# Kernel optimization log

Measured on AMD Instinct MI355X. Metric: run time of the kernel, lower is better.

The kernel has to match this reference:

```python
import jax, jax.numpy as jnp
import numpy as np

NUM_LEVELS = 4
N = 524288


def _e8_roots() -> np.ndarray:
    """The 240 roots of the E8 lattice, float32 [240, 8].

    Type 1 (112): all permutations of (+-1, +-1, 0^6).
    Type 2 (128): (+-1/2)^8 with an even number of minus signs.
    """
    roots = []
    for i in range(8):
        for j in range(i + 1, 8):
            for si in (1.0, -1.0):
                for sj in (1.0, -1.0):
                    v = np.zeros(8, dtype=np.float64)
                    v[i] = si
                    v[j] = sj
                    roots.append(v)
    for m in range(256):
        signs = np.array([1.0 if ((m >> k) & 1) == 0 else -1.0 for k in range(8)])
        if int((signs < 0).sum()) % 2 == 0:
            roots.append(0.5 * signs)
    out = np.stack(roots).astype(np.float32)
    assert out.shape == (240, 8)
    return out


def setup_inputs() -> dict:
    key = jax.random.key(0)
    x = jax.random.normal(key, (N, 8), dtype=jnp.float32)
    roots = jnp.asarray(_e8_roots())  # [240, 8] fixed codebook (buffer)
    return {"x": x, "roots": roots}


def reference(x, roots):
    # Residual multi-level nearest-neighbor quantization against E8 roots.
    x_flat = x.reshape(-1, 8)                       # [N, 8]
    r2 = jnp.sum(roots * roots, axis=1)[None, :]    # [1, 240]
    qsum = jnp.zeros_like(x_flat)
    residual = x_flat
    indices = []
    for _level in range(NUM_LEVELS):
        res2 = jnp.sum(residual * residual, axis=1, keepdims=True)      # [N, 1]
        # squared euclidean distances, clamped at 0 for numerical safety
        d2 = jnp.clip(res2 + r2 - 2.0 * (residual @ roots.T), 0.0)      # [N, 240]
        idx = jnp.argmin(d2, axis=-1)                                   # [N]
        qsum = qsum + roots[idx]                                        # gather
        residual = x_flat - qsum
        indices.append(idx)
    quantized = qsum.reshape(x.shape)
    # straight-through estimator: value == quantized, grad flows via x
    quantized_ste = quantized + x - jax.lax.stop_gradient(x)
    qerr = jnp.mean(
        (jax.lax.stop_gradient(x) - jax.lax.stop_gradient(quantized)) ** 2
    )
    idx_stack = jnp.stack(indices).reshape((NUM_LEVELS,) + x.shape[:-1])
    return quantized_ste, idx_stack, qerr
```

## Files before the change

kernel.cpp:

```cpp
#include <hip/hip_runtime.h>
#include <math.h>


__global__ __launch_bounds__(256) void e8_quant_kernel(
    const float* __restrict__ x, const float* __restrict__ roots,
    float* __restrict__ out, float* __restrict__ partials, int nrow) {
#pragma clang fp contract(off)
  __shared__ float lroots[240 * 8];
  __shared__ float wred0[4];
  __shared__ float wred1[4];
  for (int t = threadIdx.x; t < 240 * 8; t += 256) lroots[t] = roots[t];
  __syncthreads();

  const int row0 = blockIdx.x * 512 + threadIdx.x;
  const int row1 = row0 + 256;
  const bool act0 = row0 < nrow;
  const bool act1 = row1 < nrow;
  float* out_idx = out + (size_t)nrow * 8;

  float xr0[8], qs0[8], r0[8];
  float xr1[8], qs1[8], r1[8];
  float e0 = 0.f, e1 = 0.f;

  if (act0) {
    const float4 xa = *(const float4*)(x + (size_t)row0 * 8);
    const float4 xb = *(const float4*)(x + (size_t)row0 * 8 + 4);
    xr0[0] = xa.x; xr0[1] = xa.y; xr0[2] = xa.z; xr0[3] = xa.w;
    xr0[4] = xb.x; xr0[5] = xb.y; xr0[6] = xb.z; xr0[7] = xb.w;
#pragma unroll
    for (int k = 0; k < 8; ++k) { qs0[k] = 0.f; r0[k] = xr0[k]; }
  }
  if (act1) {
    const float4 xa = *(const float4*)(x + (size_t)row1 * 8);
    const float4 xb = *(const float4*)(x + (size_t)row1 * 8 + 4);
    xr1[0] = xa.x; xr1[1] = xa.y; xr1[2] = xa.z; xr1[3] = xa.w;
    xr1[4] = xb.x; xr1[5] = xb.y; xr1[6] = xb.z; xr1[7] = xb.w;
#pragma unroll
    for (int k = 0; k < 8; ++k) { qs1[k] = 0.f; r1[k] = xr1[k]; }
  }

  auto level_step = [&](int lvl, float (&xr)[8], float (&qs)[8],
                        float (&r)[8], int row) {
    float q[8];
#pragma unroll
    for (int k = 0; k < 8; ++k) q[k] = r[k] * r[k];
    const float res2 = ((q[0] + q[1]) + (q[2] + q[3])) +
                       ((q[4] + q[5]) + (q[6] + q[7]));
    const float s = res2 + 2.0f;

    float mg[8];
    int sb[8];
#pragma unroll
    for (int k = 0; k < 8; ++k) {
      const unsigned u = __float_as_uint(r[k]);
      mg[k] = __uint_as_float(u & 0x7fffffffu);
      sb[k] = (int)(u >> 31);
    }
    const int msk = sb[0] | (sb[1] << 1) | (sb[2] << 2) | (sb[3] << 3) |
                    (sb[4] << 4) | (sb[5] << 5) | (sb[6] << 6) | (sb[7] << 7);
    const int par = __popc(msk) & 1;
    const float Sabs = ((mg[0] + mg[1]) + (mg[2] + mg[3])) +
                       ((mg[4] + mg[5]) + (mg[6] + mg[7]));

    const int K0 = 0 | (sb[0] << 3), K1 = 1 | (sb[1] << 3),
              K2 = 2 | (sb[2] << 3), K3 = 3 | (sb[3] << 3),
              K4 = 4 | (sb[4] << 3), K5 = 5 | (sb[5] << 3),
              K6 = 6 | (sb[6] << 3), K7 = 7 | (sb[7] << 3);

    const bool g01 = mg[1] > mg[0];
    const float h01 = fmaxf(mg[0], mg[1]), l01 = fminf(mg[0], mg[1]);
    const int hk01 = g01 ? K1 : K0, lk01 = g01 ? K0 : K1;
    const bool g23 = mg[3] > mg[2];
    const float h23 = fmaxf(mg[2], mg[3]), l23 = fminf(mg[2], mg[3]);
    const int hk23 = g23 ? K3 : K2, lk23 = g23 ? K2 : K3;
    const bool g45 = mg[5] > mg[4];
    const float h45 = fmaxf(mg[4], mg[5]), l45 = fminf(mg[4], mg[5]);
    const int hk45 = g45 ? K5 : K4, lk45 = g45 ? K4 : K5;
    const bool g67 = mg[7] > mg[6];
    const float h67 = fmaxf(mg[6], mg[7]), l67 = fminf(mg[6], mg[7]);
    const int hk67 = g67 ? K7 : K6, lk67 = g67 ? K6 : K7;
    const bool qg0 = h23 > h01;
    const float qh0 = fmaxf(h01, h23);
    const int qhk0 = qg0 ? hk23 : hk01;
    const float sA0 = qg0 ? l23 : l01;
    const int sAk0 = qg0 ? lk23 : lk01;
    const float sB0 = qg0 ? h01 : h23;
    const int sBk0 = qg0 ? hk01 : hk23;
    const float loL0 = qg0 ? l01 : l23;
    const bool qx0 = sB0 > sA0;
    const float qs0v = fmaxf(sA0, sB0);
    const int qsk0 = qx0 ? sBk0 : sAk0;
    const float qt0 = qx0 ? fmaxf(sA0, loL0) : sB0;
    const bool qg1 = h67 > h45;
    const float qh1 = fmaxf(h45, h67);
    const int qhk1 = qg1 ? hk67 : hk45;
    const float sA1 = qg1 ? l67 : l45;
    const int sAk1 = qg1 ? lk67 : lk45;
    const float sB1 = qg1 ? h45 : h67;
    const int sBk1 = qg1 ? hk45 : hk67;
    const float loL1 = qg1 ? l45 : l67;
    const bool qx1 = sB1 > sA1;
    const float qs1v = fmaxf(sA1, sB1);
    const int qsk1 = qx1 ? sBk1 : sAk1;
    const float qt1 = qx1 ? fmaxf(sA1, loL1) : sB1;
    const bool fg = qh1 > qh0;
    const float A1v = fmaxf(qh0, qh1);
    const int A1K = fg ? qhk1 : qhk0;
    const float fA = fg ? qs1v : qs0v;
    const int fAk = fg ? qsk1 : qsk0;
    const float fB = fg ? qh0 : qh1;
    const int fBk = fg ? qhk0 : qhk1;
    const float tW = fg ? qt1 : qt0;
    const float sL = fg ? qs0v : qs1v;
    const bool fh = fB > fA;
    const float A2v = fmaxf(fA, fB);
    const int A2K = fh ? fBk : fAk;
    const float A3v = fh ? fmaxf(fA, sL) : fmaxf(tW, fB);

    const bool n0 = l23 < l01;
    const float mn0 = fminf(l01, l23);
    const int mnk0 = n0 ? lk23 : lk01;
    const float pr0 = n0 ? h23 : h01;
    const float ot0 = fmaxf(l01, l23);
    const bool n1 = l67 < l45;
    const float mn1 = fminf(l45, l67);
    const int mnk1 = n1 ? lk67 : lk45;
    const float pr1 = n1 ? h67 : h45;
    const float ot1 = fmaxf(l45, l67);
    const bool nf = mn1 < mn0;
    const float Aminv = fminf(mn0, mn1);
    const int AminK = nf ? mnk1 : mnk0;
    const float prW = nf ? pr1 : pr0;
    const float otW = nf ? ot1 : ot0;
    const float mnL = fmaxf(mn0, mn1);
    const float Amin2v = fminf(prW, fminf(otW, mnL));

    const float dT1r = A1v + A2v;
    const float halfS = 0.5f * Sabs;
    const float dT2 = par ? (halfS - Aminv) : halfS;

    const int p1 = A1K & 7, p2 = A2K & 7;
    const int s1b = A1K >> 3, s2b = A2K >> 3;
    const bool o12 = p1 < p2;
    const int imn = o12 ? p1 : p2, jmx = o12 ? p2 : p1;
    const int sIb = o12 ? s1b : s2b, sJb = o12 ? s2b : s1b;
    const int pbase = imn * 7 - ((imn * (imn - 1)) >> 1) + (jmx - imn - 1);
    const int t1idx = (pbase << 2) | (sIb << 1) | sJb;

    const int mp = AminK & 7;
    const int mf = par ? (msk ^ (1 << mp)) : msk;
    const int t2idx = 112 + (mf >> 1);

    const float thr = (res2 + 2.0f * Sabs + 2.0f) * 0x1.0p-20f;
    const bool a1 = (A2v - A3v) > thr;
    const bool a2 = par ? ((Amin2v - Aminv) > thr)
                        : ((Aminv + Amin2v) > thr);
    const bool c = fabsf(dT1r - dT2) > thr;

    float d1 = fmaf(-2.f, dT1r, s);
    int i1 = t1idx;
    float d2x = 0.f;
    int i2 = t2idx;

    if (__any(!a1)) {
      if (!a1) {
        if (Aminv > thr) {
          float best = 3.4028235e38f;
          int bidx = 0;
          int ci = 0;
#pragma unroll
          for (int i = 0; i < 8; ++i) {
#pragma unroll
            for (int j = i + 1; j < 8; ++j) {
              const float aa = mg[i] + mg[j];
              const float d = fmaf(-2.f, aa, s);
              const int idx = (ci << 2) | (sb[i] << 1) | sb[j];
              if (d < best) { best = d; bidx = idx; }
              ++ci;
            }
          }
          d1 = best;
          i1 = bidx;
        } else {
          float best = 3.4028235e38f;
          int be = 0;
          int ci = 0;
#pragma unroll
          for (int i = 0; i < 8; ++i) {
#pragma unroll
            for (int j = i + 1; j < 8; ++j) {
              const float a = r[i] + r[j];
              const float b = r[i] - r[j];
              float d;
              d = fmaf(-2.f, a, s);
              if (d < best) { best = d; be = ci + 0; }
              d = fmaf(-2.f, b, s);
              if (d < best) { best = d; be = ci + 1; }
              d = fmaf(2.f, b, s);
              if (d < best) { best = d; be = ci + 2; }
              d = fmaf(2.f, a, s);
              if (d < best) { best = d; be = ci + 3; }
              ci += 4;
            }
          }
          d1 = best;
          i1 = be;
        }
      }
    }

    if (__any(!a2)) {
      if (!a2) {
        float h[8];
#pragma unroll
        for (int k = 0; k < 8; ++k) h[k] = 0.5f * r[k];
        const bool cheap = par && ((Amin2v + Amin2v) > thr);
        if (cheap) {
          float best2 = 3.4028235e38f;
          int bt = 0;
#pragma unroll
          for (int k = 0; k < 8; ++k) {
            const int mk = msk ^ (1 << k);
            float v = (mk & 1) ? -h[0] : h[0];
#pragma unroll
            for (int j = 1; j < 8; ++j)
              v = (mk & (1 << j)) ? (v - h[j]) : (v + h[j]);
            const float d = fmaf(-2.f, v, s);
            const int t = mk >> 1;
            const bool take = (d < best2) || (d == best2 && t < bt);
            best2 = take ? d : best2;
            bt = take ? t : bt;
          }
          d2x = best2;
          i2 = 112 + bt;
        } else {
          float best2 = 3.4028235e38f;
          int bt = 0;
#pragma unroll 1
          for (int t = 0; t < 128; ++t) {
            const int m = (t << 1) | (__popc(t) & 1);
            float v = (m & 1) ? -h[0] : h[0];
#pragma unroll
            for (int j = 1; j < 8; ++j)
              v = (m & (1 << j)) ? (v - h[j]) : (v + h[j]);
            const float d = fmaf(-2.f, v, s);
            if (d < best2) { best2 = d; bt = t; }
          }
          d2x = best2;
          i2 = 112 + bt;
        }
      }
    }

    if (__any(!c && a2)) {
      if (!c && a2) {
        const int flip = par ? mp : 8;
        float v = (flip == 0) ? -(0.5f * mg[0]) : (0.5f * mg[0]);
#pragma unroll
        for (int j = 1; j < 8; ++j) {
          const float tj = 0.5f * mg[j];
          v = (flip == j) ? (v - tj) : (v + tj);
        }
        d2x = fmaf(-2.f, v, s);
      }
    }

    const int bi = c ? ((dT1r > dT2) ? i1 : i2)
                     : ((d1 <= d2x) ? i1 : i2);

    out_idx[(size_t)lvl * nrow + row] = (float)bi;

    const float4 ra = *(const float4*)(lroots + bi * 8);
    const float4 rb = *(const float4*)(lroots + bi * 8 + 4);
    qs[0] += ra.x; qs[1] += ra.y; qs[2] += ra.z; qs[3] += ra.w;
    qs[4] += rb.x; qs[5] += rb.y; qs[6] += rb.z; qs[7] += rb.w;
#pragma unroll
    for (int k = 0; k < 8; ++k) r[k] = xr[k] - qs[k];
  };

#pragma unroll 1
  for (int lvl = 0; lvl < 4; ++lvl) {
    if (act0) level_step(lvl, xr0, qs0, r0, row0);
    if (act1) level_step(lvl, xr1, qs1, r1, row1);
  }

  if (act0) {
    float o[8];
#pragma unroll
    for (int k = 0; k < 8; ++k) o[k] = (qs0[k] + xr0[k]) - xr0[k];
    *(float4*)(out + (size_t)row0 * 8) = make_float4(o[0], o[1], o[2], o[3]);
    *(float4*)(out + (size_t)row0 * 8 + 4) =
        make_float4(o[4], o[5], o[6], o[7]);
#pragma unroll
    for (int k = 0; k < 8; ++k) e0 = fmaf(r0[k], r0[k], e0);
  }
  if (act1) {
    float o[8];
#pragma unroll
    for (int k = 0; k < 8; ++k) o[k] = (qs1[k] + xr1[k]) - xr1[k];
    *(float4*)(out + (size_t)row1 * 8) = make_float4(o[0], o[1], o[2], o[3]);
    *(float4*)(out + (size_t)row1 * 8 + 4) =
        make_float4(o[4], o[5], o[6], o[7]);
#pragma unroll
    for (int k = 0; k < 8; ++k) e1 = fmaf(r1[k], r1[k], e1);
  }

#pragma unroll
  for (int off = 32; off > 0; off >>= 1) e0 += __shfl_down(e0, off, 64);
#pragma unroll
  for (int off = 32; off > 0; off >>= 1) e1 += __shfl_down(e1, off, 64);
  const int lane = threadIdx.x & 63, wv = threadIdx.x >> 6;
  if (lane == 0) { wred0[wv] = e0; wred1[wv] = e1; }
  __syncthreads();
  if (threadIdx.x == 0) {
    partials[2 * blockIdx.x] =
        (wred0[0] + wred0[1]) + (wred0[2] + wred0[3]);
    partials[2 * blockIdx.x + 1] =
        (wred1[0] + wred1[1]) + (wred1[2] + wred1[3]);
  }
}

__global__ __launch_bounds__(256) void qerr_reduce_kernel(
    const float* __restrict__ partials, float* __restrict__ out, int n,
    size_t pos, float scale) {
#pragma clang fp contract(off)
  __shared__ float wred[4];
  float e = 0.f;
  for (int i = threadIdx.x; i < n; i += 256) e += partials[i];
#pragma unroll
  for (int off = 32; off > 0; off >>= 1) e += __shfl_down(e, off, 64);
  const int lane = threadIdx.x & 63, wv = threadIdx.x >> 6;
  if (lane == 0) wred[wv] = e;
  __syncthreads();
  if (threadIdx.x == 0)
    out[pos] = ((wred[0] + wred[1]) + (wred[2] + wred[3])) * scale;
}

extern "C" void kernel_launch(void* const* d_in, const int* in_sizes, int n_in,
                              void* d_out, int out_size, void* d_ws,
                              size_t ws_size, hipStream_t stream) {
  const float* x = (const float*)d_in[0];
  const float* roots = (const float*)d_in[1];
  float* out = (float*)d_out;
  float* partials = (float*)d_ws;

  const int nrow = in_sizes[0] / 8;
  const int nblocks = (nrow + 511) / 512;

  e8_quant_kernel<<<nblocks, 256, 0, stream>>>(x, roots, out, partials, nrow);

  const size_t qerr_pos = (size_t)nrow * 12;
  const float scale = 1.0f / (float)((size_t)nrow * 8);
  qerr_reduce_kernel<<<1, 256, 0, stream>>>(partials, out, 2 * nblocks,
                                            qerr_pos, scale);
}
```

Measured before the change: 90.28 us.

## Drop shared-memory codebook and rebuild chosen root arithmetically, merging both rows' slow paths

```diff
diff --git a/kernel.cpp b/kernel.cpp
--- a/kernel.cpp
+++ b/kernel.cpp
@@ -6,317 +6,348 @@
     const float* __restrict__ x, const float* __restrict__ roots,
     float* __restrict__ out, float* __restrict__ partials, int nrow) {
 #pragma clang fp contract(off)
-  __shared__ float lroots[240 * 8];
-  __shared__ float wred0[4];
-  __shared__ float wred1[4];
-  for (int t = threadIdx.x; t < 240 * 8; t += 256) lroots[t] = roots[t];
-  __syncthreads();
+  __shared__ float wredA[4];
+  __shared__ float wredB[4];
 
   const int row0 = blockIdx.x * 512 + threadIdx.x;
   const int row1 = row0 + 256;
-  const bool act0 = row0 < nrow;
-  const bool act1 = row1 < nrow;
+  const bool act[2] = {row0 < nrow, row1 < nrow};
+  const int rl[2] = {act[0] ? row0 : nrow - 1, act[1] ? row1 : nrow - 1};
   float* out_idx = out + (size_t)nrow * 8;
-
-  float xr0[8], qs0[8], r0[8];
-  float xr1[8], qs1[8], r1[8];
-  float e0 = 0.f, e1 = 0.f;
-
-  if (act0) {
-    const float4 xa = *(const float4*)(x + (size_t)row0 * 8);
-    const float4 xb = *(const float4*)(x + (size_t)row0 * 8 + 4);
-    xr0[0] = xa.x; xr0[1] = xa.y; xr0[2] = xa.z; xr0[3] = xa.w;
-    xr0[4] = xb.x; xr0[5] = xb.y; xr0[6] = xb.z; xr0[7] = xb.w;
-#pragma unroll
-    for (int k = 0; k < 8; ++k) { qs0[k] = 0.f; r0[k] = xr0[k]; }
+  float* op[2] = {out_idx + row0, out_idx + row1};
+
+  float xr[2][8], qs[2][8], rr[2][8];
+#pragma unroll
+  for (int sl = 0; sl < 2; ++sl) {
+    const float4 xa = *(const float4*)(x + (size_t)rl[sl] * 8);
+    const float4 xb = *(const float4*)(x + (size_t)rl[sl] * 8 + 4);
+    xr[sl][0] = xa.x; xr[sl][1] = xa.y; xr[sl][2] = xa.z; xr[sl][3] = xa.w;
+    xr[sl][4] = xb.x; xr[sl][5] = xb.y; xr[sl][6] = xb.z; xr[sl][7] = xb.w;
+#pragma unroll
+    for (int k = 0; k < 8; ++k) { qs[sl][k] = 0.f; rr[sl][k] = xr[sl][k]; }
   }
-  if (act1) {
-    const float4 xa = *(const float4*)(x + (size_t)row1 * 8);
-    const float4 xb = *(const float4*)(x + (size_t)row1 * 8 + 4);
-    xr1[0] = xa.x; xr1[1] = xa.y; xr1[2] = xa.z; xr1[3] = xa.w;
-    xr1[4] = xb.x; xr1[5] = xb.y; xr1[6] = xb.z; xr1[7] = xb.w;
-#pragma unroll
-    for (int k = 0; k < 8; ++k) { qs1[k] = 0.f; r1[k] = xr1[k]; }
-  }
-
-  auto level_step = [&](int lvl, float (&xr)[8], float (&qs)[8],
-                        float (&r)[8], int row) {
-    float q[8];
-#pragma unroll
-    for (int k = 0; k < 8; ++k) q[k] = r[k] * r[k];
-    const float res2 = ((q[0] + q[1]) + (q[2] + q[3])) +
-                       ((q[4] + q[5]) + (q[6] + q[7]));
-    const float s = res2 + 2.0f;
-
-    float mg[8];
-    int sb[8];
-#pragma unroll
-    for (int k = 0; k < 8; ++k) {
-      const unsigned u = __float_as_uint(r[k]);
-      mg[k] = __uint_as_float(u & 0x7fffffffu);
-      sb[k] = (int)(u >> 31);
+
+#pragma unroll 1
+  for (int lvl = 0; lvl < 4; ++lvl) {
+    float s_[2], thr_[2], dT1_[2], dT2_[2], Amn_[2], Amn2_[2];
+    int t1_[2], t2_[2], pk_[2], bi_[2];
+    bool a1_[2], a2_[2], c_[2], fell_[2], pT1_[2];
+
+#pragma unroll
+    for (int sl = 0; sl < 2; ++sl) {
+      float q[8];
+#pragma unroll
+      for (int k = 0; k < 8; ++k) q[k] = rr[sl][k] * rr[sl][k];
+      const float res2 = ((q[0] + q[1]) + (q[2] + q[3])) +
+                         ((q[4] + q[5]) + (q[6] + q[7]));
+      const float s = res2 + 2.0f;
+
+      float mg[8];
+      int sb[8];
+#pragma unroll
+      for (int k = 0; k < 8; ++k) {
+        const unsigned u = __float_as_uint(rr[sl][k]);
+        mg[k] = __uint_as_float(u & 0x7fffffffu);
+        sb[k] = (int)(u >> 31);
+      }
+      const int msk = sb[0] | (sb[1] << 1) | (sb[2] << 2) | (sb[3] << 3) |
+                      (sb[4] << 4) | (sb[5] << 5) | (sb[6] << 6) |
+                      (sb[7] << 7);
+      const int par = __popc(msk) & 1;
+      const float Sabs = ((mg[0] + mg[1]) + (mg[2] + mg[3])) +
+                         ((mg[4] + mg[5]) + (mg[6] + mg[7]));
+
+      const int K0 = 0 | (sb[0] << 3), K1 = 1 | (sb[1] << 3),
+                K2 = 2 | (sb[2] << 3), K3 = 3 | (sb[3] << 3),
+                K4 = 4 | (sb[4] << 3), K5 = 5 | (sb[5] << 3),
+                K6 = 6 | (sb[6] << 3), K7 = 7 | (sb[7] << 3);
+
+      const bool g01 = mg[1] > mg[0];
+      const float h01 = fmaxf(mg[0], mg[1]), l01 = fminf(mg[0], mg[1]);
+      const int hk01 = g01 ? K1 : K0, lk01 = g01 ? K0 : K1;
+      const bool g23 = mg[3] > mg[2];
+      const float h23 = fmaxf(mg[2], mg[3]), l23 = fminf(mg[2], mg[3]);
+      const int hk23 = g23 ? K3 : K2, lk23 = g23 ? K2 : K3;
+      const bool g45 = mg[5] > mg[4];
+      const float h45 = fmaxf(mg[4], mg[5]), l45 = fminf(mg[4], mg[5]);
+      const int hk45 = g45 ? K5 : K4, lk45 = g45 ? K4 : K5;
+      const bool g67 = mg[7] > mg[6];
+      const float h67 = fmaxf(mg[6], mg[7]), l67 = fminf(mg[6], mg[7]);
+      const int hk67 = g67 ? K7 : K6, lk67 = g67 ? K6 : K7;
+      const bool qg0 = h23 > h01;
+      const float qh0 = fmaxf(h01, h23);
+      const int qhk0 = qg0 ? hk23 : hk01;
+      const float sA0 = qg0 ? l23 : l01;
+      const int sAk0 = qg0 ? lk23 : lk01;
+      const float sB0 = qg0 ? h01 : h23;
+      const int sBk0 = qg0 ? hk01 : hk23;
+      const float loL0 = qg0 ? l01 : l23;
+      const bool qx0 = sB0 > sA0;
+      const float qs0v = fmaxf(sA0, sB0);
+      const int qsk0 = qx0 ? sBk0 : sAk0;
+      const float qt0 = qx0 ? fmaxf(sA0, loL0) : sB0;
+      const bool qg1 = h67 > h45;
+      const float qh1 = fmaxf(h45, h67);
+      const int qhk1 = qg1 ? hk67 : hk45;
+      const float sA1 = qg1 ? l67 : l45;
+      const int sAk1 = qg1 ? lk67 : lk45;
+      const float sB1 = qg1 ? h45 : h67;
+      const int sBk1 = qg1 ? hk45 : hk67;
+      const float loL1 = qg1 ? l45 : l67;
+      const bool qx1 = sB1 > sA1;
+      const float qs1v = fmaxf(sA1, sB1);
+      const int qsk1 = qx1 ? sBk1 : sAk1;
+      const float qt1 = qx1 ? fmaxf(sA1, loL1) : sB1;
+      const bool fg = qh1 > qh0;
+      const float A1v = fmaxf(qh0, qh1);
+      const int A1K = fg ? qhk1 : qhk0;
+      const float fA = fg ? qs1v : qs0v;
+      const int fAk = fg ? qsk1 : qsk0;
+      const float fB = fg ? qh0 : qh1;
+      const int fBk = fg ? qhk0 : qhk1;
+      const float tW = fg ? qt1 : qt0;
+      const float sL = fg ? qs0v : qs1v;
+      const bool fh = fB > fA;
+      const float A2v = fmaxf(fA, fB);
+      const int A2K = fh ? fBk : fAk;
+      const float A3v = fh ? fmaxf(fA, sL) : fmaxf(tW, fB);
+
+      const bool n0 = l23 < l01;
+      const float mn0 = fminf(l01, l23);
+      const int mnk0 = n0 ? lk23 : lk01;
+      const float pr0 = n0 ? h23 : h01;
+      const float ot0 = fmaxf(l01, l23);
+      const bool n1 = l67 < l45;
+      const float mn1 = fminf(l45, l67);
+      const int mnk1 = n1 ? lk67 : lk45;
+      const float pr1 = n1 ? h67 : h45;
+      const float ot1 = fmaxf(l45, l67);
+      const bool nf = mn1 < mn0;
+      const float Aminv = fminf(mn0, mn1);
+      const int AminK = nf ? mnk1 : mnk0;
+      const float prW = nf ? pr1 : pr0;
+      const float otW = nf ? ot1 : ot0;
+      const float mnL = fmaxf(mn0, mn1);
+      const float Amin2v = fminf(prW, fminf(otW, mnL));
+
+      const float dT1r = A1v + A2v;
+      const float halfS = 0.5f * Sabs;
+      const float dT2 = par ? (halfS - Aminv) : halfS;
+
+      const int p1 = A1K & 7, p2 = A2K & 7;
+      const int s1b = A1K >> 3, s2b = A2K >> 3;
+      const bool o12 = p1 < p2;
+      const int imn = o12 ? p1 : p2, jmx = o12 ? p2 : p1;
+      const int sIb = o12 ? s1b : s2b, sJb = o12 ? s2b : s1b;
+      const int pbase = imn * 7 - ((imn * (imn - 1)) >> 1) + (jmx - imn - 1);
+      const int t1idx = (pbase << 2) | (sIb << 1) | sJb;
+
+      const int mp = AminK & 7;
+      const int mf = par ? (msk ^ (1 << mp)) : msk;
+      const int t2idx = 112 + (mf >> 1);
+
+      const float thr = (res2 + 2.0f * Sabs + 2.0f) * 0x1.0p-20f;
+      const bool a1 = (A2v - A3v) > thr;
+      const bool a2 = par ? ((Amin2v - Aminv) > thr)
+                          : ((Aminv + Amin2v) > thr);
+      const bool c = fabsf(dT1r - dT2) > thr;
+
+      const int one = (1 << imn) | (1 << jmx);
+      const int sm1 = (sIb << imn) | (sJb << jmx);
+
+      s_[sl] = s; thr_[sl] = thr; dT1_[sl] = dT1r; dT2_[sl] = dT2;
+      Amn_[sl] = Aminv; Amn2_[sl] = Amin2v;
+      t1_[sl] = t1idx; t2_[sl] = t2idx;
+      pk_[sl] = one | (sm1 << 8) | (mf << 16) | (mp << 24);
+      a1_[sl] = a1; a2_[sl] = a2; c_[sl] = c;
+      const bool pT1 = dT1r > dT2;
+      pT1_[sl] = pT1;
+      bi_[sl] = pT1 ? t1idx : t2idx;
+      fell_[sl] = false;
     }
-    const int msk = sb[0] | (sb[1] << 1) | (sb[2] << 2) | (sb[3] << 3) |
-                    (sb[4] << 4) | (sb[5] << 5) | (sb[6] << 6) | (sb[7] << 7);
-    const int par = __popc(msk) & 1;
-    const float Sabs = ((mg[0] + mg[1]) + (mg[2] + mg[3])) +
-                       ((mg[4] + mg[5]) + (mg[6] + mg[7]));
-
-    const int K0 = 0 | (sb[0] << 3), K1 = 1 | (sb[1] << 3),
-              K2 = 2 | (sb[2] << 3), K3 = 3 | (sb[3] << 3),
-              K4 = 4 | (sb[4] << 3), K5 = 5 | (sb[5] << 3),
-              K6 = 6 | (sb[6] << 3), K7 = 7 | (sb[7] << 3);
-
-    const bool g01 = mg[1] > mg[0];
-    const float h01 = fmaxf(mg[0], mg[1]), l01 = fminf(mg[0], mg[1]);
-    const int hk01 = g01 ? K1 : K0, lk01 = g01 ? K0 : K1;
-    const bool g23 = mg[3] > mg[2];
-    const float h23 = fmaxf(mg[2], mg[3]), l23 = fminf(mg[2], mg[3]);
-    const int hk23 = g23 ? K3 : K2, lk23 = g23 ? K2 : K3;
-    const bool g45 = mg[5] > mg[4];
-    const float h45 = fmaxf(mg[4], mg[5]), l45 = fminf(mg[4], mg[5]);
-    const int hk45 = g45 ? K5 : K4, lk45 = g45 ? K4 : K5;
-    const bool g67 = mg[7] > mg[6];
-    const float h67 = fmaxf(mg[6], mg[7]), l67 = fminf(mg[6], mg[7]);
-    const int hk67 = g67 ? K7 : K6, lk67 = g67 ? K6 : K7;
-    const bool qg0 = h23 > h01;
-    const float qh0 = fmaxf(h01, h23);
-    const int qhk0 = qg0 ? hk23 : hk01;
-    const float sA0 = qg0 ? l23 : l01;
-    const int sAk0 = qg0 ? lk23 : lk01;
-    const float sB0 = qg0 ? h01 : h23;
-    const int sBk0 = qg0 ? hk01 : hk23;
-    const float loL0 = qg0 ? l01 : l23;
-    const bool qx0 = sB0 > sA0;
-    const float qs0v = fmaxf(sA0, sB0);
-    const int qsk0 = qx0 ? sBk0 : sAk0;
-    const float qt0 = qx0 ? fmaxf(sA0, loL0) : sB0;
-    const bool qg1 = h67 > h45;
-    const float qh1 = fmaxf(h45, h67);
-    const int qhk1 = qg1 ? hk67 : hk45;
-    const float sA1 = qg1 ? l67 : l45;
-    const int sAk1 = qg1 ? lk67 : lk45;
-    const float sB1 = qg1 ? h45 : h67;
-    const int sBk1 = qg1 ? hk45 : hk67;
-    const float loL1 = qg1 ? l45 : l67;
-    const bool qx1 = sB1 > sA1;
-    const float qs1v = fmaxf(sA1, sB1);
-    const int qsk1 = qx1 ? sBk1 : sAk1;
-    const float qt1 = qx1 ? fmaxf(sA1, loL1) : sB1;
-    const bool fg = qh1 > qh0;
-    const float A1v = fmaxf(qh0, qh1);
-    const int A1K = fg ? qhk1 : qhk0;
-    const float fA = fg ? qs1v : qs0v;
-    const int fAk = fg ? qsk1 : qsk0;
-    const float fB = fg ? qh0 : qh1;
-    const int fBk = fg ? qhk0 : qhk1;
-    const float tW = fg ? qt1 : qt0;
-    const float sL = fg ? qs0v : qs1v;
-    const bool fh = fB > fA;
-    const float A2v = fmaxf(fA, fB);
-    const int A2K = fh ? fBk : fAk;
-    const float A3v = fh ? fmaxf(fA, sL) : fmaxf(tW, fB);
-
-    const bool n0 = l23 < l01;
-    const float mn0 = fminf(l01, l23);
-    const int mnk0 = n0 ? lk23 : lk01;
-    const float pr0 = n0 ? h23 : h01;
-    const float ot0 = fmaxf(l01, l23);
-    const bool n1 = l67 < l45;
-    const float mn1 = fminf(l45, l67);
-    const int mnk1 = n1 ? lk67 : lk45;
-    const float pr1 = n1 ? h67 : h45;
-    const float ot1 = fmaxf(l45, l67);
-    const bool nf = mn1 < mn0;
-    const float Aminv = fminf(mn0, mn1);
-    const int AminK = nf ? mnk1 : mnk0;
-    const float prW = nf ? pr1 : pr0;
-    const float otW = nf ? ot1 : ot0;
-    const float mnL = fmaxf(mn0, mn1);
-    const float Amin2v = fminf(prW, fminf(otW, mnL));
-
-    const float dT1r = A1v + A2v;
-    const float halfS = 0.5f * Sabs;
-    const float dT2 = par ? (halfS - Aminv) : halfS;
-
-    const int p1 = A1K & 7, p2 = A2K & 7;
-    const int s1b = A1K >> 3, s2b = A2K >> 3;
-    const bool o12 = p1 < p2;
-    const int imn = o12 ? p1 : p2, jmx = o12 ? p2 : p1;
-    const int sIb = o12 ? s1b : s2b, sJb = o12 ? s2b : s1b;
-    const int pbase = imn * 7 - ((imn * (imn - 1)) >> 1) + (jmx - imn - 1);
-    const int t1idx = (pbase << 2) | (sIb << 1) | sJb;
-
-    const int mp = AminK & 7;
-    const int mf = par ? (msk ^ (1 << mp)) : msk;
-    const int t2idx = 112 + (mf >> 1);
-
-    const float thr = (res2 + 2.0f * Sabs + 2.0f) * 0x1.0p-20f;
-    const bool a1 = (A2v - A3v) > thr;
-    const bool a2 = par ? ((Amin2v - Aminv) > thr)
-                        : ((Aminv + Amin2v) > thr);
-    const bool c = fabsf(dT1r - dT2) > thr;
-
-    float d1 = fmaf(-2.f, dT1r, s);
-    int i1 = t1idx;
-    float d2x = 0.f;
-    int i2 = t2idx;
-
-    if (__any(!a1)) {
-      if (!a1) {
-        if (Aminv > thr) {
-          float best = 3.4028235e38f;
-          int bidx = 0;
-          int ci = 0;
-#pragma unroll
-          for (int i = 0; i < 8; ++i) {
-#pragma unroll
-            for (int j = i + 1; j < 8; ++j) {
-              const float aa = mg[i] + mg[j];
-              const float d = fmaf(-2.f, aa, s);
-              const int idx = (ci << 2) | (sb[i] << 1) | sb[j];
-              if (d < best) { best = d; bidx = idx; }
-              ++ci;
+
+    const bool slowAny = (!a1_[0]) | (!a2_[0]) | (!c_[0]) |
+                         (!a1_[1]) | (!a2_[1]) | (!c_[1]);
+    if (__any(slowAny)) {
+#pragma unroll
+      for (int sl = 0; sl < 2; ++sl) {
+        const bool slow = (!a1_[sl]) | (!a2_[sl]) | (!c_[sl]);
+        if (slow) {
+          float mg[8], h[8];
+          int sb[8];
+#pragma unroll
+          for (int k = 0; k < 8; ++k) {
+            const unsigned u = __float_as_uint(rr[sl][k]);
+            mg[k] = __uint_as_float(u & 0x7fffffffu);
+            sb[k] = (int)(u >> 31);
+            h[k] = 0.5f * rr[sl][k];
+          }
+          const int msk = sb[0] | (sb[1] << 1) | (sb[2] << 2) |
+                          (sb[3] << 3) | (sb[4] << 4) | (sb[5] << 5) |
+                          (sb[6] << 6) | (sb[7] << 7);
+          const int par = __popc(msk) & 1;
+          const float s = s_[sl];
+
+          float d1v = fmaf(-2.f, dT1_[sl], s);
+          int i1v = t1_[sl];
+          if (!a1_[sl]) {
+            if (Amn_[sl] > thr_[sl]) {
+              float best = 3.4028235e38f;
+              int bidx = 0, ci = 0;
+#pragma unroll 1
+              for (int i = 0; i < 8; ++i) {
+#pragma unroll 1
+                for (int j = i + 1; j < 8; ++j) {
+                  const float aa = mg[i] + mg[j];
+                  const float d = fmaf(-2.f, aa, s);
+                  const int idx = (ci << 2) | (sb[i] << 1) | sb[j];
+                  if (d < best) { best = d; bidx = idx; }
+                  ++ci;
+                }
+              }
+              d1v = best; i1v = bidx;
+            } else {
+              float best = 3.4028235e38f;
+              int be = 0, ci = 0;
+#pragma unroll 1
+              for (int i = 0; i < 8; ++i) {
+#pragma unroll 1
+                for (int j = i + 1; j < 8; ++j) {
+                  const float a = rr[sl][i] + rr[sl][j];
+                  const float b = rr[sl][i] - rr[sl][j];
+                  float d;
+                  d = fmaf(-2.f, a, s);
+                  if (d < best) { best = d; be = ci + 0; }
+                  d = fmaf(-2.f, b, s);
+                  if (d < best) { best = d; be = ci + 1; }
+                  d = fmaf(2.f, b, s);
+                  if (d < best) { best = d; be = ci + 2; }
+                  d = fmaf(2.f, a, s);
+                  if (d < best) { best = d; be = ci + 3; }
+                  ci += 4;
+                }
+              }
+              d1v = best; i1v = be;
             }
           }
-          d1 = best;
-          i1 = bidx;
-        } else {
-          float best = 3.4028235e38f;
-          int be = 0;
-          int ci = 0;
-#pragma unroll
-          for (int i = 0; i < 8; ++i) {
-#pragma unroll
-            for (int j = i + 1; j < 8; ++j) {
-              const float a = r[i] + r[j];
-              const float b = r[i] - r[j];
-              float d;
-              d = fmaf(-2.f, a, s);
-              if (d < best) { best = d; be = ci + 0; }
-              d = fmaf(-2.f, b, s);
-              if (d < best) { best = d; be = ci + 1; }
-              d = fmaf(2.f, b, s);
-              if (d < best) { best = d; be = ci + 2; }
-              d = fmaf(2.f, a, s);
-              if (d < best) { best = d; be = ci + 3; }
-              ci += 4;
+
+          float d2v = 0.f;
+          int i2v = t2_[sl];
+          if (!a2_[sl]) {
+            const bool cheap = par && ((Amn2_[sl] + Amn2_[sl]) > thr_[sl]);
+            if (cheap) {
+              float best2 = 3.4028235e38f;
+              int bt = 0;
+#pragma unroll 1
+              for (int k = 0; k < 8; ++k) {
+                const int mk = msk ^ (1 << k);
+                float v = (mk & 1) ? -h[0] : h[0];
+#pragma unroll
+                for (int j = 1; j < 8; ++j)
+                  v = (mk & (1 << j)) ? (v - h[j]) : (v + h[j]);
+                const float d = fmaf(-2.f, v, s);
+                const int t = mk >> 1;
+                const bool take = (d < best2) || (d == best2 && t < bt);
+                best2 = take ? d : best2;
+                bt = take ? t : bt;
+              }
+              d2v = best2; i2v = 112 + bt;
+            } else {
+              float best2 = 3.4028235e38f;
+              int bt = 0;
+#pragma unroll 1
+              for (int t = 0; t < 128; ++t) {
+                const int m = (t << 1) | (__popc(t) & 1);
+                float v = (m & 1) ? -h[0] : h[0];
+#pragma unroll
+                for (int j = 1; j < 8; ++j)
+                  v = (m & (1 << j)) ? (v - h[j]) : (v + h[j]);
+                const float d = fmaf(-2.f, v, s);
+                if (d < best2) { best2 = d; bt = t; }
+              }
+              d2v = best2; i2v = 112 + bt;
             }
+          } else if (!c_[sl]) {
+            const int mp = (pk_[sl] >> 24) & 7;
+            const int flip = par ? mp : 8;
+            float v = (flip == 0) ? -(0.5f * mg[0]) : (0.5f * mg[0]);
+#pragma unroll
+            for (int j = 1; j < 8; ++j) {
+              const float tj = 0.5f * mg[j];
+              v = (flip == j) ? (v - tj) : (v + tj);
+            }
+            d2v = fmaf(-2.f, v, s);
           }
-          d1 = best;
-          i1 = be;
+
+          const bool pT1 = c_[sl] ? (dT1_[sl] > dT2_[sl]) : (d1v <= d2v);
+          pT1_[sl] = pT1;
+          bi_[sl] = pT1 ? i1v : i2v;
+          const bool fl = (!a1_[sl]) | (!a2_[sl]);
+          fell_[sl] = fl;
+          if (fl) {
+            const float4 ra = *(const float4*)(roots + (size_t)bi_[sl] * 8);
+            const float4 rb =
+                *(const float4*)(roots + (size_t)bi_[sl] * 8 + 4);
+            qs[sl][0] += ra.x; qs[sl][1] += ra.y;
+            qs[sl][2] += ra.z; qs[sl][3] += ra.w;
+            qs[sl][4] += rb.x; qs[sl][5] += rb.y;
+            qs[sl][6] += rb.z; qs[sl][7] += rb.w;
+#pragma unroll
+            for (int k = 0; k < 8; ++k) rr[sl][k] = xr[sl][k] - qs[sl][k];
+          }
         }
       }
     }
 
-    if (__any(!a2)) {
-      if (!a2) {
-        float h[8];
-#pragma unroll
-        for (int k = 0; k < 8; ++k) h[k] = 0.5f * r[k];
-        const bool cheap = par && ((Amin2v + Amin2v) > thr);
-        if (cheap) {
-          float best2 = 3.4028235e38f;
-          int bt = 0;
-#pragma unroll
-          for (int k = 0; k < 8; ++k) {
-            const int mk = msk ^ (1 << k);
-            float v = (mk & 1) ? -h[0] : h[0];
-#pragma unroll
-            for (int j = 1; j < 8; ++j)
-              v = (mk & (1 << j)) ? (v - h[j]) : (v + h[j]);
-            const float d = fmaf(-2.f, v, s);
-            const int t = mk >> 1;
-            const bool take = (d < best2) || (d == best2 && t < bt);
-            best2 = take ? d : best2;
-            bt = take ? t : bt;
-          }
-          d2x = best2;
-          i2 = 112 + bt;
-        } else {
-          float best2 = 3.4028235e38f;
-          int bt = 0;
-#pragma unroll 1
-          for (int t = 0; t < 128; ++t) {
-            const int m = (t << 1) | (__popc(t) & 1);
-            float v = (m & 1) ? -h[0] : h[0];
-#pragma unroll
-            for (int j = 1; j < 8; ++j)
-              v = (m & (1 << j)) ? (v - h[j]) : (v + h[j]);
-            const float d = fmaf(-2.f, v, s);
-            if (d < best2) { best2 = d; bt = t; }
-          }
-          d2x = best2;
-          i2 = 112 + bt;
+#pragma unroll
+    for (int sl = 0; sl < 2; ++sl) {
+      if (act[sl]) *op[sl] = (float)bi_[sl];
+      op[sl] += nrow;
+      if (!fell_[sl]) {
+        const int one = pk_[sl] & 0xFF;
+        const int sm1 = (pk_[sl] >> 8) & 0xFF;
+        const int mfv = (pk_[sl] >> 16) & 0xFF;
+#pragma unroll
+        for (int k = 0; k < 8; ++k) {
+          const float t1r =
+              ((one >> k) & 1) ? (((sm1 >> k) & 1) ? -1.f : 1.f) : 0.f;
+          const float t2r = ((mfv >> k) & 1) ? -0.5f : 0.5f;
+          qs[sl][k] += pT1_[sl] ? t1r : t2r;
         }
+#pragma unroll
+        for (int k = 0; k < 8; ++k) rr[sl][k] = xr[sl][k] - qs[sl][k];
       }
     }
-
-    if (__any(!c && a2)) {
-      if (!c && a2) {
-        const int flip = par ? mp : 8;
-        float v = (flip == 0) ? -(0.5f * mg[0]) : (0.5f * mg[0]);
-#pragma unroll
-        for (int j = 1; j < 8; ++j) {
-          const float tj = 0.5f * mg[j];
-          v = (flip == j) ? (v - tj) : (v + tj);
-        }
-        d2x = fmaf(-2.f, v, s);
-      }
+  }
+
+  float e[2] = {0.f, 0.f};
+#pragma unroll
+  for (int sl = 0; sl < 2; ++sl) {
+    if (act[sl]) {
+      float o[8];
+#pragma unroll
+      for (int k = 0; k < 8; ++k) o[k] = (qs[sl][k] + xr[sl][k]) - xr[sl][k];
+      const int rw = sl ? row1 : row0;
+      *(float4*)(out + (size_t)rw * 8) = make_float4(o[0], o[1], o[2], o[3]);
+      *(float4*)(out + (size_t)rw * 8 + 4) =
+          make_float4(o[4], o[5], o[6], o[7]);
+#pragma unroll
+      for (int k = 0; k < 8; ++k) e[sl] = fmaf(rr[sl][k], rr[sl][k], e[sl]);
     }
-
-    const int bi = c ? ((dT1r > dT2) ? i1 : i2)
-                     : ((d1 <= d2x) ? i1 : i2);
-
-    out_idx[(size_t)lvl * nrow + row] = (float)bi;
-
-    const float4 ra = *(const float4*)(lroots + bi * 8);
-    const float4 rb = *(const float4*)(lroots + bi * 8 + 4);
-    qs[0] += ra.x; qs[1] += ra.y; qs[2] += ra.z; qs[3] += ra.w;
-    qs[4] += rb.x; qs[5] += rb.y; qs[6] += rb.z; qs[7] += rb.w;
-#pragma unroll
-    for (int k = 0; k < 8; ++k) r[k] = xr[k] - qs[k];
-  };
-
-#pragma unroll 1
-  for (int lvl = 0; lvl < 4; ++lvl) {
-    if (act0) level_step(lvl, xr0, qs0, r0, row0);
-    if (act1) level_step(lvl, xr1, qs1, r1, row1);
   }
 
-  if (act0) {
-    float o[8];
-#pragma unroll
-    for (int k = 0; k < 8; ++k) o[k] = (qs0[k] + xr0[k]) - xr0[k];
-    *(float4*)(out + (size_t)row0 * 8) = make_float4(o[0], o[1], o[2], o[3]);
-    *(float4*)(out + (size_t)row0 * 8 + 4) =
-        make_float4(o[4], o[5], o[6], o[7]);
-#pragma unroll
-    for (int k = 0; k < 8; ++k) e0 = fmaf(r0[k], r0[k], e0);
-  }
-  if (act1) {
-    float o[8];
-#pragma unroll
-    for (int k = 0; k < 8; ++k) o[k] = (qs1[k] + xr1[k]) - xr1[k];
-    *(float4*)(out + (size_t)row1 * 8) = make_float4(o[0], o[1], o[2], o[3]);
-    *(float4*)(out + (size_t)row1 * 8 + 4) =
-        make_float4(o[4], o[5], o[6], o[7]);
-#pragma unroll
-    for (int k = 0; k < 8; ++k) e1 = fmaf(r1[k], r1[k], e1);
-  }
-
+  float e0 = e[0], e1 = e[1];
 #pragma unroll
   for (int off = 32; off > 0; off >>= 1) e0 += __shfl_down(e0, off, 64);
 #pragma unroll
   for (int off = 32; off > 0; off >>= 1) e1 += __shfl_down(e1, off, 64);
   const int lane = threadIdx.x & 63, wv = threadIdx.x >> 6;
-  if (lane == 0) { wred0[wv] = e0; wred1[wv] = e1; }
+  if (lane == 0) { wredA[wv] = e0; wredB[wv] = e1; }
   __syncthreads();
   if (threadIdx.x == 0) {
-    partials[2 * blockIdx.x] =
-        (wred0[0] + wred0[1]) + (wred0[2] + wred0[3]);
+    partials[2 * blockIdx.x] = (wredA[0] + wredA[1]) + (wredA[2] + wredA[3]);
     partials[2 * blockIdx.x + 1] =
-        (wred1[0] + wred1[1]) + (wred1[2] + wred1[3]);
+        (wredB[0] + wredB[1]) + (wredB[2] + wredB[3]);
   }
 }
 
```

New measurement: 97.78 us. 8.3% more time.

## Process one row per thread and drop shared-memory roots table

Applied to the files above, without the earlier changes.

```diff
diff --git a/kernel.cpp b/kernel.cpp
--- a/kernel.cpp
+++ b/kernel.cpp
@@ -6,44 +6,28 @@
     const float* __restrict__ x, const float* __restrict__ roots,
     float* __restrict__ out, float* __restrict__ partials, int nrow) {
 #pragma clang fp contract(off)
-  __shared__ float lroots[240 * 8];
-  __shared__ float wred0[4];
-  __shared__ float wred1[4];
-  for (int t = threadIdx.x; t < 240 * 8; t += 256) lroots[t] = roots[t];
-  __syncthreads();
-
-  const int row0 = blockIdx.x * 512 + threadIdx.x;
-  const int row1 = row0 + 256;
-  const bool act0 = row0 < nrow;
-  const bool act1 = row1 < nrow;
+  __shared__ float wred[4];
+
+  const int row = blockIdx.x * 256 + threadIdx.x;
+  const bool act = row < nrow;
+  const int rl = act ? row : nrow - 1;
   float* out_idx = out + (size_t)nrow * 8;
 
-  float xr0[8], qs0[8], r0[8];
-  float xr1[8], qs1[8], r1[8];
-  float e0 = 0.f, e1 = 0.f;
-
-  if (act0) {
-    const float4 xa = *(const float4*)(x + (size_t)row0 * 8);
-    const float4 xb = *(const float4*)(x + (size_t)row0 * 8 + 4);
-    xr0[0] = xa.x; xr0[1] = xa.y; xr0[2] = xa.z; xr0[3] = xa.w;
-    xr0[4] = xb.x; xr0[5] = xb.y; xr0[6] = xb.z; xr0[7] = xb.w;
-#pragma unroll
-    for (int k = 0; k < 8; ++k) { qs0[k] = 0.f; r0[k] = xr0[k]; }
+  float xr[8], qs[8], rr[8];
+  {
+    const float4 xa = *(const float4*)(x + (size_t)rl * 8);
+    const float4 xb = *(const float4*)(x + (size_t)rl * 8 + 4);
+    xr[0] = xa.x; xr[1] = xa.y; xr[2] = xa.z; xr[3] = xa.w;
+    xr[4] = xb.x; xr[5] = xb.y; xr[6] = xb.z; xr[7] = xb.w;
+#pragma unroll
+    for (int k = 0; k < 8; ++k) { qs[k] = 0.f; rr[k] = xr[k]; }
   }
-  if (act1) {
-    const float4 xa = *(const float4*)(x + (size_t)row1 * 8);
-    const float4 xb = *(const float4*)(x + (size_t)row1 * 8 + 4);
-    xr1[0] = xa.x; xr1[1] = xa.y; xr1[2] = xa.z; xr1[3] = xa.w;
-    xr1[4] = xb.x; xr1[5] = xb.y; xr1[6] = xb.z; xr1[7] = xb.w;
-#pragma unroll
-    for (int k = 0; k < 8; ++k) { qs1[k] = 0.f; r1[k] = xr1[k]; }
-  }
-
-  auto level_step = [&](int lvl, float (&xr)[8], float (&qs)[8],
-                        float (&r)[8], int row) {
+
+#pragma unroll 1
+  for (int lvl = 0; lvl < 4; ++lvl) {
     float q[8];
 #pragma unroll
-    for (int k = 0; k < 8; ++k) q[k] = r[k] * r[k];
+    for (int k = 0; k < 8; ++k) q[k] = rr[k] * rr[k];
     const float res2 = ((q[0] + q[1]) + (q[2] + q[3])) +
                        ((q[4] + q[5]) + (q[6] + q[7]));
     const float s = res2 + 2.0f;
@@ -52,7 +36,7 @@
     int sb[8];
 #pragma unroll
     for (int k = 0; k < 8; ++k) {
-      const unsigned u = __float_as_uint(r[k]);
+      const unsigned u = __float_as_uint(rr[k]);
       mg[k] = __uint_as_float(u & 0x7fffffffu);
       sb[k] = (int)(u >> 31);
     }
@@ -157,167 +141,154 @@
                         : ((Aminv + Amin2v) > thr);
     const bool c = fabsf(dT1r - dT2) > thr;
 
-    float d1 = fmaf(-2.f, dT1r, s);
-    int i1 = t1idx;
-    float d2x = 0.f;
-    int i2 = t2idx;
-
-    if (__any(!a1)) {
-      if (!a1) {
-        if (Aminv > thr) {
-          float best = 3.4028235e38f;
-          int bidx = 0;
-          int ci = 0;
-#pragma unroll
-          for (int i = 0; i < 8; ++i) {
-#pragma unroll
-            for (int j = i + 1; j < 8; ++j) {
-              const float aa = mg[i] + mg[j];
-              const float d = fmaf(-2.f, aa, s);
-              const int idx = (ci << 2) | (sb[i] << 1) | sb[j];
-              if (d < best) { best = d; bidx = idx; }
-              ++ci;
+    bool pT1 = dT1r > dT2;
+    int bi = pT1 ? t1idx : t2idx;
+    bool fell = false;
+
+    const bool slow = (!a1) | (!a2) | (!c);
+    if (__any(slow)) {
+      if (slow) {
+        float h[8];
+#pragma unroll
+        for (int k = 0; k < 8; ++k) h[k] = 0.5f * rr[k];
+
+        float d1v = fmaf(-2.f, dT1r, s);
+        int i1v = t1idx;
+        if (!a1) {
+          if (Aminv > thr) {
+            float best = 3.4028235e38f;
+            int bidx = 0, ci = 0;
+#pragma unroll
+            for (int i = 0; i < 8; ++i) {
+#pragma unroll
+              for (int j = i + 1; j < 8; ++j) {
+                const float aa = mg[i] + mg[j];
+                const float d = fmaf(-2.f, aa, s);
+                const int idx = (ci << 2) | (sb[i] << 1) | sb[j];
+                if (d < best) { best = d; bidx = idx; }
+                ++ci;
+              }
             }
+            d1v = best; i1v = bidx;
+          } else {
+            float best = 3.4028235e38f;
+            int be = 0, ci = 0;
+#pragma unroll
+            for (int i = 0; i < 8; ++i) {
+#pragma unroll
+              for (int j = i + 1; j < 8; ++j) {
+                const float a = rr[i] + rr[j];
+                const float b = rr[i] - rr[j];
+                float d;
+                d = fmaf(-2.f, a, s);
+                if (d < best) { best = d; be = ci + 0; }
+                d = fmaf(-2.f, b, s);
+                if (d < best) { best = d; be = ci + 1; }
+                d = fmaf(2.f, b, s);
+                if (d < best) { best = d; be = ci + 2; }
+                d = fmaf(2.f, a, s);
+                if (d < best) { best = d; be = ci + 3; }
+                ci += 4;
+              }
+            }
+            d1v = best; i1v = be;
           }
-          d1 = best;
-          i1 = bidx;
-        } else {
-          float best = 3.4028235e38f;
-          int be = 0;
-          int ci = 0;
-#pragma unroll
-          for (int i = 0; i < 8; ++i) {
-#pragma unroll
-            for (int j = i + 1; j < 8; ++j) {
-              const float a = r[i] + r[j];
-              const float b = r[i] - r[j];
-              float d;
-              d = fmaf(-2.f, a, s);
-              if (d < best) { best = d; be = ci + 0; }
-              d = fmaf(-2.f, b, s);
-              if (d < best) { best = d; be = ci + 1; }
-              d = fmaf(2.f, b, s);
-              if (d < best) { best = d; be = ci + 2; }
-              d = fmaf(2.f, a, s);
-              if (d < best) { best = d; be = ci + 3; }
-              ci += 4;
+        }
+
+        float d2v = 0.f;
+        int i2v = t2idx;
+        if (!a2) {
+          const bool cheap = par && ((Amin2v + Amin2v) > thr);
+          if (cheap) {
+            float best2 = 3.4028235e38f;
+            int bt = 0;
+#pragma unroll
+            for (int k = 0; k < 8; ++k) {
+              const int mk = msk ^ (1 << k);
+              float v = (mk & 1) ? -h[0] : h[0];
+#pragma unroll
+              for (int j = 1; j < 8; ++j)
+                v = (mk & (1 << j)) ? (v - h[j]) : (v + h[j]);
+              const float d = fmaf(-2.f, v, s);
+              const int t = mk >> 1;
+              const bool take = (d < best2) || (d == best2 && t < bt);
+              best2 = take ? d : best2;
+              bt = take ? t : bt;
             }
+            d2v = best2; i2v = 112 + bt;
+          } else {
+            float best2 = 3.4028235e38f;
+            int bt = 0;
+#pragma unroll 1
+            for (int t = 0; t < 128; ++t) {
+              const int m = (t << 1) | (__popc(t) & 1);
+              float v = (m & 1) ? -h[0] : h[0];
+#pragma unroll
+              for (int j = 1; j < 8; ++j)
+                v = (m & (1 << j)) ? (v - h[j]) : (v + h[j]);
+              const float d = fmaf(-2.f, v, s);
+              if (d < best2) { best2 = d; bt = t; }
+            }
+            d2v = best2; i2v = 112 + bt;
           }
-          d1 = best;
-          i1 = be;
+        } else if (!c) {
+          const int flip = par ? mp : 8;
+          float v = (flip == 0) ? -(0.5f * mg[0]) : (0.5f * mg[0]);
+#pragma unroll
+          for (int j = 1; j < 8; ++j) {
+            const float tj = 0.5f * mg[j];
+            v = (flip == j) ? (v - tj) : (v + tj);
+          }
+          d2v = fmaf(-2.f, v, s);
+        }
+
+        pT1 = c ? (dT1r > dT2) : (d1v <= d2v);
+        bi = pT1 ? i1v : i2v;
+        fell = (!a1) | (!a2);
+        if (fell) {
+          const float4 ra = *(const float4*)(roots + (size_t)bi * 8);
+          const float4 rb = *(const float4*)(roots + (size_t)bi * 8 + 4);
+          qs[0] += ra.x; qs[1] += ra.y; qs[2] += ra.z; qs[3] += ra.w;
+          qs[4] += rb.x; qs[5] += rb.y; qs[6] += rb.z; qs[7] += rb.w;
+#pragma unroll
+          for (int k = 0; k < 8; ++k) rr[k] = xr[k] - qs[k];
         }
       }
     }
 
-    if (__any(!a2)) {
-      if (!a2) {
-        float h[8];
-#pragma unroll
-        for (int k = 0; k < 8; ++k) h[k] = 0.5f * r[k];
-        const bool cheap = par && ((Amin2v + Amin2v) > thr);
-        if (cheap) {
-          float best2 = 3.4028235e38f;
-          int bt = 0;
-#pragma unroll
-          for (int k = 0; k < 8; ++k) {
-            const int mk = msk ^ (1 << k);
-            float v = (mk & 1) ? -h[0] : h[0];
-#pragma unroll
-            for (int j = 1; j < 8; ++j)
-              v = (mk & (1 << j)) ? (v - h[j]) : (v + h[j]);
-            const float d = fmaf(-2.f, v, s);
-            const int t = mk >> 1;
-            const bool take = (d < best2) || (d == best2 && t < bt);
-            best2 = take ? d : best2;
-            bt = take ? t : bt;
-          }
-          d2x = best2;
-          i2 = 112 + bt;
-        } else {
-          float best2 = 3.4028235e38f;
-          int bt = 0;
-#pragma unroll 1
-          for (int t = 0; t < 128; ++t) {
-            const int m = (t << 1) | (__popc(t) & 1);
-            float v = (m & 1) ? -h[0] : h[0];
-#pragma unroll
-            for (int j = 1; j < 8; ++j)
-              v = (m & (1 << j)) ? (v - h[j]) : (v + h[j]);
-            const float d = fmaf(-2.f, v, s);
-            if (d < best2) { best2 = d; bt = t; }
-          }
-          d2x = best2;
-          i2 = 112 + bt;
-        }
+    if (act) out_idx[(size_t)lvl * nrow + row] = (float)bi;
+
+    if (!fell) {
+#pragma unroll
+      for (int k = 0; k < 8; ++k) {
+        const float t1r = (k == imn) ? (sIb ? -1.f : 1.f)
+                                     : ((k == jmx) ? (sJb ? -1.f : 1.f) : 0.f);
+        const float t2r = ((mf >> k) & 1) ? -0.5f : 0.5f;
+        qs[k] += pT1 ? t1r : t2r;
       }
+#pragma unroll
+      for (int k = 0; k < 8; ++k) rr[k] = xr[k] - qs[k];
     }
-
-    if (__any(!c && a2)) {
-      if (!c && a2) {
-        const int flip = par ? mp : 8;
-        float v = (flip == 0) ? -(0.5f * mg[0]) : (0.5f * mg[0]);
-#pragma unroll
-        for (int j = 1; j < 8; ++j) {
-          const float tj = 0.5f * mg[j];
-          v = (flip == j) ? (v - tj) : (v + tj);
-        }
-        d2x = fmaf(-2.f, v, s);
-      }
-    }
-
-    const int bi = c ? ((dT1r > dT2) ? i1 : i2)
-                     : ((d1 <= d2x) ? i1 : i2);
-
-    out_idx[(size_t)lvl * nrow + row] = (float)bi;
-
-    const float4 ra = *(const float4*)(lroots + bi * 8);
-    const float4 rb = *(const float4*)(lroots + bi * 8 + 4);
-    qs[0] += ra.x; qs[1] += ra.y; qs[2] += ra.z; qs[3] += ra.w;
-    qs[4] += rb.x; qs[5] += rb.y; qs[6] += rb.z; qs[7] += rb.w;
-#pragma unroll
-    for (int k = 0; k < 8; ++k) r[k] = xr[k] - qs[k];
-  };
-
-#pragma unroll 1
-  for (int lvl = 0; lvl < 4; ++lvl) {
-    if (act0) level_step(lvl, xr0, qs0, r0, row0);
-    if (act1) level_step(lvl, xr1, qs1, r1, row1);
   }
 
-  if (act0) {
+  float e = 0.f;
+  if (act) {
     float o[8];
 #pragma unroll
-    for (int k = 0; k < 8; ++k) o[k] = (qs0[k] + xr0[k]) - xr0[k];
-    *(float4*)(out + (size_t)row0 * 8) = make_float4(o[0], o[1], o[2], o[3]);
-    *(float4*)(out + (size_t)row0 * 8 + 4) =
-        make_float4(o[4], o[5], o[6], o[7]);
-#pragma unroll
-    for (int k = 0; k < 8; ++k) e0 = fmaf(r0[k], r0[k], e0);
+    for (int k = 0; k < 8; ++k) o[k] = (qs[k] + xr[k]) - xr[k];
+    *(float4*)(out + (size_t)row * 8) = make_float4(o[0], o[1], o[2], o[3]);
+    *(float4*)(out + (size_t)row * 8 + 4) = make_float4(o[4], o[5], o[6], o[7]);
+#pragma unroll
+    for (int k = 0; k < 8; ++k) e = fmaf(rr[k], rr[k], e);
   }
-  if (act1) {
-    float o[8];
-#pragma unroll
-    for (int k = 0; k < 8; ++k) o[k] = (qs1[k] + xr1[k]) - xr1[k];
-    *(float4*)(out + (size_t)row1 * 8) = make_float4(o[0], o[1], o[2], o[3]);
-    *(float4*)(out + (size_t)row1 * 8 + 4) =
-        make_float4(o[4], o[5], o[6], o[7]);
-#pragma unroll
-    for (int k = 0; k < 8; ++k) e1 = fmaf(r1[k], r1[k], e1);
-  }
-
-#pragma unroll
-  for (int off = 32; off > 0; off >>= 1) e0 += __shfl_down(e0, off, 64);
-#pragma unroll
-  for (int off = 32; off > 0; off >>= 1) e1 += __shfl_down(e1, off, 64);
+
+#pragma unroll
+  for (int off = 32; off > 0; off >>= 1) e += __shfl_down(e, off, 64);
   const int lane = threadIdx.x & 63, wv = threadIdx.x >> 6;
-  if (lane == 0) { wred0[wv] = e0; wred1[wv] = e1; }
+  if (lane == 0) wred[wv] = e;
   __syncthreads();
-  if (threadIdx.x == 0) {
-    partials[2 * blockIdx.x] =
-        (wred0[0] + wred0[1]) + (wred0[2] + wred0[3]);
-    partials[2 * blockIdx.x + 1] =
-        (wred1[0] + wred1[1]) + (wred1[2] + wred1[3]);
-  }
+  if (threadIdx.x == 0)
+    partials[blockIdx.x] = (wred[0] + wred[1]) + (wred[2] + wred[3]);
 }
 
 __global__ __launch_bounds__(256) void qerr_reduce_kernel(
@@ -345,12 +316,12 @@
   float* partials = (float*)d_ws;
 
   const int nrow = in_sizes[0] / 8;
-  const int nblocks = (nrow + 511) / 512;
+  const int nblocks = (nrow + 255) / 256;
 
   e8_quant_kernel<<<nblocks, 256, 0, stream>>>(x, roots, out, partials, nrow);
 
   const size_t qerr_pos = (size_t)nrow * 12;
   const float scale = 1.0f / (float)((size_t)nrow * 8);
-  qerr_reduce_kernel<<<1, 256, 0, stream>>>(partials, out, 2 * nblocks,
-                                            qerr_pos, scale);
+  qerr_reduce_kernel<<<1, 256, 0, stream>>>(partials, out, nblocks, qerr_pos,
+                                            scale);
 }
```

New measurement: 88.54 us, median of 2. No clear change (-1.9%).
